# Kernel tuning notes

Measured on AMD Instinct MI355X. Metric: run time of the kernel, lower is better.

The kernel has to match this reference:

```python
import jax, jax.numpy as jnp
import numpy as np

HID = 128
K = 8
G = 1024        # number of graphs (jets)
N_SV = 16       # secondary vertices per graph
N_TRK = 64      # tracks per graph


def _mlp2(x, W1, b1, W2, b2):
    # Linear -> ELU -> Linear -> ReLU (the sv/trk encoders)
    h = jax.nn.elu(x @ W1 + b1)
    return jax.nn.relu(h @ W2 + b2)


def _dynamic_edge_conv(src, dst, W, b, k):
    # DynamicEdgeConv with bipartite input (x_src, x_dst):
    #   edge_index = knn(src, dst, k) per graph (Euclidean in feature space)
    #   message    = nn(cat([x_i, x_j - x_i]))  with x_i = dst(target), x_j = src(neighbor)
    #   aggr       = max over the k neighbors of each target
    # src: [G, Ns, D], dst: [G, Nq, D]
    dots = jnp.einsum('gqd,gsd->gqs', dst, src)
    d2 = (jnp.sum(dst * dst, -1)[:, :, None] - 2.0 * dots
          + jnp.sum(src * src, -1)[:, None, :])            # [G, Nq, Ns]
    _, idx = jax.lax.top_k(-d2, k)                          # k nearest sources, [G, Nq, k]
    xj = jax.vmap(lambda s, i: s[i])(src, idx)              # gather neighbors [G, Nq, k, D]
    xi = dst[:, :, None, :]                                 # [G, Nq, 1, D]
    edge_feat = jnp.concatenate([jnp.broadcast_to(xi, xj.shape), xj - xi], axis=-1)
    msg = jax.nn.elu(edge_feat @ W + b)                     # [G, Nq, k, D]
    return jnp.max(msg, axis=2)                             # max-scatter -> [G, Nq, D]


def setup_inputs() -> dict:
    key = jax.random.key(0)
    ks = jax.random.split(key, 16)
    s = 0.05
    inp = {
        'x_sv': jax.random.normal(ks[0], (G * N_SV, 2), jnp.float32),
        'x_trk': jax.random.normal(ks[1], (G * N_TRK, 8), jnp.float32),
        # sv encoder
        'W_sv1': jax.random.normal(ks[2], (2, HID), jnp.float32) * s,
        'b_sv1': jnp.zeros((HID,), jnp.float32),
        'W_sv2': jax.random.normal(ks[3], (HID, HID), jnp.float32) * s,
        'b_sv2': jnp.zeros((HID,), jnp.float32),
        # trk encoder
        'W_trk1': jax.random.normal(ks[4], (8, HID), jnp.float32) * s,
        'b_trk1': jnp.zeros((HID,), jnp.float32),
        'W_trk2': jax.random.normal(ks[5], (HID, HID), jnp.float32) * s,
        'b_trk2': jnp.zeros((HID,), jnp.float32),
        # edge-conv MLPs (Linear(2*HID, HID) + ELU)
        'W_c1': jax.random.normal(ks[6], (2 * HID, HID), jnp.float32) * s,
        'b_c1': jnp.zeros((HID,), jnp.float32),
        'W_c2': jax.random.normal(ks[7], (2 * HID, HID), jnp.float32) * s,
        'b_c2': jnp.zeros((HID,), jnp.float32),
        # output head 128->64->32->4->1
        'W_o1': jax.random.normal(ks[8], (HID, 64), jnp.float32) * s,
        'b_o1': jnp.zeros((64,), jnp.float32),
        'W_o2': jax.random.normal(ks[9], (64, 32), jnp.float32) * s,
        'b_o2': jnp.zeros((32,), jnp.float32),
        'W_o3': jax.random.normal(ks[10], (32, 4), jnp.float32) * s,
        'b_o3': jnp.zeros((4,), jnp.float32),
        'W_o4': jax.random.normal(ks[11], (4, 1), jnp.float32) * s,
        'b_o4': jnp.zeros((1,), jnp.float32),
        # block-structured batch assignment (sorted, equal-size graphs)
        'batch_sv': jnp.arange(G * N_SV, dtype=jnp.int64 if jax.config.jax_enable_x64 else jnp.int32) // N_SV,
        'batch_trk': jnp.arange(G * N_TRK, dtype=jnp.int64 if jax.config.jax_enable_x64 else jnp.int32) // N_TRK,
    }
    return inp


def reference(x_sv, x_trk, W_sv1, b_sv1, W_sv2, b_sv2, W_trk1, b_trk1, W_trk2, b_trk2,
              W_c1, b_c1, W_c2, b_c2, W_o1, b_o1, W_o2, b_o2, W_o3, b_o3, W_o4, b_o4,
              batch_sv, batch_trk):
    # Batches are equal-size contiguous blocks (see setup_inputs), so per-graph
    # knn/gather/max are expressed as batched ops over a leading G dimension.
    sv = _mlp2(x_sv, W_sv1, b_sv1, W_sv2, b_sv2).reshape(G, N_SV, HID)
    trk = _mlp2(x_trk, W_trk1, b_trk1, W_trk2, b_trk2).reshape(G, N_TRK, HID)
    # conv_1: sources = encoded SVs, targets = encoded tracks
    f1 = _dynamic_edge_conv(sv, trk, W_c1, b_c1, K)          # [G, N_TRK, HID]
    # conv_2: sources = f1 (per-track), targets = encoded tracks
    f2 = _dynamic_edge_conv(f1, trk, W_c2, b_c2, K)          # [G, N_TRK, HID]
    # avg_pool_x with cluster == batch: mean over tracks of each graph
    pooled = jnp.mean(f2, axis=1)                            # [G, HID]
    h = jax.nn.elu(pooled @ W_o1 + b_o1)
    h = jax.nn.elu(h @ W_o2 + b_o2)
    h = jax.nn.elu(h @ W_o3 + b_o3)
    out = h @ W_o4 + b_o4                                    # [G, 1]
    batch = jnp.arange(G)
    return out, batch
```

## Files before the change

### kernel.cpp

```cpp
#include <hip/hip_runtime.h>

#define G_    1024
#define TPB   512
#define INF_F 3.4e38f

typedef __attribute__((ext_vector_type(8))) short short8;
typedef __attribute__((ext_vector_type(4))) float f32x4;

__device__ __forceinline__ float elu_fast(float x) { return x > 0.f ? x : __expf(x) - 1.f; }
__device__ __forceinline__ float elu_ref(float x)  { return x > 0.f ? x : expm1f(x); }

#define ROT(r, d)    ((r)*128 + (((d) + 4*(r)) & 127))
#define BS1(s, c)    (2048 + (s)*128 + (((c) + 4*(s)) & 127))

#define FMA4(acc_, sc_, wv_) do { (acc_).x = fmaf((sc_),(wv_).x,(acc_).x); \
                                  (acc_).y = fmaf((sc_),(wv_).y,(acc_).y); \
                                  (acc_).z = fmaf((sc_),(wv_).z,(acc_).z); \
                                  (acc_).w = fmaf((sc_),(wv_).w,(acc_).w); } while(0)
#define MAX4(mm_, bb_)       do { (mm_).x = fmaxf((mm_).x,(bb_).x); \
                                  (mm_).y = fmaxf((mm_).y,(bb_).y); \
                                  (mm_).z = fmaxf((mm_).z,(bb_).z); \
                                  (mm_).w = fmaxf((mm_).w,(bb_).w); } while(0)

#define MFMA1(acc_, A_, B_) \
    acc_ = __builtin_amdgcn_mfma_f32_16x16x32_bf16((A_), (B_), (acc_), 0, 0, 0)

union U8 { unsigned d[4]; short8 v; };

__device__ __forceinline__ short8 pack_frag(const float* p0, const float* p1) {
    float xs[8];
    *(float4*)&xs[0] = *(const float4*)p0;
    *(float4*)&xs[4] = *(const float4*)p1;
    U8 uo;
    #pragma unroll
    for (int k = 0; k < 4; k++) {
        unsigned u0 = __float_as_uint(xs[2 * k]);
        unsigned u1 = __float_as_uint(xs[2 * k + 1]);
        u0 = u0 + 0x7FFFu + ((u0 >> 16) & 1u);
        u1 = u1 + 0x7FFFu + ((u1 >> 16) & 1u);
        uo.d[k] = (u0 >> 16) | (u1 & 0xFFFF0000u);
    }
    return uo.v;
}

__device__ __forceinline__ unsigned short bf16_of(float v) {
    unsigned u = __float_as_uint(v);
    u = u + 0x7FFFu + ((u >> 16) & 1u);
    return (unsigned short)(u >> 16);
}
__device__ __forceinline__ float f32_of(unsigned short h) {
    return __uint_as_float((unsigned)h << 16);
}

__global__ void prep_pack(const float* __restrict__ Wtrk2, const float* __restrict__ Wsv2,
                          const float* __restrict__ Wc1,   const float* __restrict__ Wc2,
                          unsigned short* __restrict__ wsu) {
    const int o = blockIdx.x * 256 + threadIdx.x;
    if (o >= 6 * 16384) return;
    const int m = o >> 14, pos = o & 16383;
    const int j = pos & 7, lane = (pos >> 3) & 63, tile = pos >> 9;
    const int ks = tile >> 3, ni = tile & 7;
    const int d = ks * 32 + (lane >> 4) * 8 + j;
    const int c = ni * 16 + (lane & 15);
    const int e = d * 128 + c;
    float v;
    switch (m) {
        case 0: v = Wtrk2[e]; break;
        case 1: v = Wsv2[e]; break;
        case 2: v = Wc1[16384 + e]; break;
        case 3: v = Wc1[e] - Wc1[16384 + e]; break;
        case 4: v = Wc2[e] - Wc2[16384 + e]; break;
        default: v = Wc2[16384 + e]; break;
    }
    wsu[m * 16384 + pos] = bf16_of(v);
}

#define LOADB1(B_, m_, pos_) B_ = *(const short8*)(wsu + (m_) * 16384 + (pos_))

__global__ __launch_bounds__(TPB, 4)
void fused_mfma(const float* __restrict__ x_sv,  const float* __restrict__ x_trk,
                const float* __restrict__ W_sv1, const float* __restrict__ b_sv1,
                const float* __restrict__ b_sv2,
                const float* __restrict__ W_trk1,const float* __restrict__ b_trk1,
                const float* __restrict__ b_trk2,
                const float* __restrict__ b_c1,  const float* __restrict__ b_c2,
                const float* __restrict__ W_o1,  const float* __restrict__ b_o1,
                const float* __restrict__ W_o2,  const float* __restrict__ b_o2,
                const float* __restrict__ W_o3,  const float* __restrict__ b_o3,
                const float* __restrict__ W_o4,  const float* __restrict__ b_o4,
                const unsigned short* __restrict__ wsu,
                float* __restrict__ out)
{
    __shared__ float sA[8192];
    __shared__ float sB[8192];
    __shared__ float sC[4096];
    unsigned* sBu = (unsigned*)sB;
    unsigned short* sCs = (unsigned short*)sC;

    const int g    = blockIdx.x;
    const int tid  = threadIdx.x;
    const int c128 = tid & 127;
    const int g4   = tid >> 7;
    const int wv   = tid >> 6;
    const int lane = tid & 63;
    const int quad = lane >> 4;
    const int ln   = lane & 15;

    sC[2048 + tid] = x_trk[(size_t)g * 512 + tid];
    if (tid < 32) sC[2560 + tid] = x_sv[(size_t)g * 32 + tid];
    __syncthreads();

    {
        float w[8];
        #pragma unroll
        for (int k = 0; k < 8; k++) w[k] = W_trk1[k * 128 + c128];
        const float b1 = b_trk1[c128];
        #pragma unroll
        for (int i = 0; i < 16; i++) {
            const int r = g4 * 16 + i;
            float xr[8];
            *(float4*)&xr[0] = *(const float4*)&sC[2048 + r * 8];
            *(float4*)&xr[4] = *(const float4*)&sC[2048 + r * 8 + 4];
            float acc = b1;
            #pragma unroll
            for (int k = 0; k < 8; k++) acc = fmaf(xr[k], w[k], acc);
            sB[ROT(r, c128)] = elu_fast(acc);
        }
    }
    __syncthreads();

    {
        const int mi = wv >> 1, nb = (wv & 1) * 4;
        const int row = mi * 16 + ln;
        f32x4 acc[4];
        #pragma unroll
        for (int t = 0; t < 4; t++) {
            const float bz = b_trk2[(nb + t) * 16 + ln];
            acc[t] = (f32x4){bz, bz, bz, bz};
        }
        #pragma unroll 1
        for (int ks = 0; ks < 4; ks++) {
            const int k0 = ks * 32 + quad * 8;
            const short8 A = pack_frag(&sB[ROT(row, k0)], &sB[ROT(row, k0 + 4)]);
            #pragma unroll
            for (int t = 0; t < 4; t++) {
                const int pos = ((ks * 8 + (nb + t)) * 64 + lane) * 8;
                short8 B;
                LOADB1(B, 0, pos);
                MFMA1(acc[t], A, B);
            }
        }
        #pragma unroll
        for (int t = 0; t < 4; t++)
            #pragma unroll
            for (int r = 0; r < 4; r++)
                sA[ROT(mi * 16 + quad * 4 + r, (nb + t) * 16 + ln)] = fmaxf(acc[t][r], 0.f);
    }
    __syncthreads();

    {
        const float w0 = W_sv1[c128], w1 = W_sv1[128 + c128];
        const float b1 = b_sv1[c128];
        #pragma unroll
        for (int i = 0; i < 4; i++) {
            const int s = g4 * 4 + i;
            sB[ROT(s, c128)] =
                elu_fast(fmaf(sC[2560 + s * 2 + 1], w1, fmaf(sC[2560 + s * 2], w0, b1)));
        }
    }
    __syncthreads();

    {
        const int ni = wv;
        const float bz = b_sv2[ni * 16 + ln];
        f32x4 acc = (f32x4){bz, bz, bz, bz};
        #pragma unroll 1
        for (int ks = 0; ks < 4; ks++) {
            const int k0 = ks * 32 + quad * 8;
            const short8 A = pack_frag(&sB[ROT(ln, k0)], &sB[ROT(ln, k0 + 4)]);
            const int pos = ((ks * 8 + ni) * 64 + lane) * 8;
            short8 B;
            LOADB1(B, 1, pos);
            MFMA1(acc, A, B);
        }
        #pragma unroll
        for (int r = 0; r < 4; r++) {
            const float v = fmaxf(acc[r], 0.f);
            sC[ROT(quad * 4 + r, ni * 16 + ln)] = v;
            float p = v * v;
            #pragma unroll
            for (int o = 1; o <= 8; o <<= 1) p += __shfl_xor(p, o, 16);
            if (ln == 0) sB[2048 + ni * 16 + quad * 4 + r] = p;
        }
    }
    __syncthreads();

    {
        const int ni = wv;
        const bool doP4 = (wv < 4);
        f32x4 accB = (f32x4){0.f, 0.f, 0.f, 0.f};
        f32x4 accS = (f32x4){0.f, 0.f, 0.f, 0.f};
        #pragma unroll 1
        for (int ks = 0; ks < 4; ks++) {
            const int k0 = ks * 32 + quad * 8;
            const short8 S = pack_frag(&sC[ROT(ln, k0)], &sC[ROT(ln, k0 + 4)]);
            const int pos = ((ks * 8 + ni) * 64 + lane) * 8;
            short8 B;
            LOADB1(B, 2, pos);
            MFMA1(accB, S, B);
            if (doP4) {
                const int row = wv * 16 + ln;
                const short8 T = pack_frag(&sA[ROT(row, k0)], &sA[ROT(row, k0 + 4)]);
                MFMA1(accS, T, S);
            }
        }
        #pragma unroll
        for (int r = 0; r < 4; r++)
            sC[BS1(quad * 4 + r, ni * 16 + ln)] = accB[r];
        if (doP4) {
            float nsv = 0.f;
            #pragma unroll
            for (int p = 0; p < 8; p++) nsv += sB[2048 + p * 16 + ln];
            #pragma unroll
            for (int r = 0; r < 4; r++)
                sB[(wv * 16 + quad * 4 + r) * 17 + ln] = fmaf(-2.f, accS[r], nsv);
        }
    }
    __syncthreads();

    {
        const int q  = tid >> 3;
        const int s0 = tid & 7;
        float sc0 = sB[q * 17 + s0];
        float sc1 = sB[q * 17 + s0 + 8];
        unsigned pack1 = 0u;
        #pragma unroll
        for (int r = 0; r < 8; r++) {
            float bv = sc0; int bs = s0;
            if (sc1 < bv) { bv = sc1; bs = s0 + 8; }
            #pragma unroll
            for (int o = 1; o <= 4; o <<= 1) {
                const float ov = __shfl_xor(bv, o, 8);
                const int   os = __shfl_xor(bs, o, 8);
                if (ov < bv || (ov == bv && os < bs)) { bv = ov; bs = os; }
            }
            pack1 |= (unsigned)bs << (4 * r);
            if (bs == s0)     sc0 = INF_F;
            if (bs == s0 + 8) sc1 = INF_F;
        }
        if (s0 == 0) sBu[1088 + q] = pack1;
    }
    __syncthreads();

    {
        const int mi = wv >> 1, nb = (wv & 1) * 4;
        const int row = mi * 16 + ln;
        f32x4 a1acc[4];
        #pragma unroll
        for (int t = 0; t < 4; t++) {
            const float bz1 = b_c1[(nb + t) * 16 + ln];
            a1acc[t] = (f32x4){bz1, bz1, bz1, bz1};
        }
        #pragma unroll 1
        for (int ks = 0; ks < 4; ks++) {
            const int k0 = ks * 32 + quad * 8;
            const short8 A = pack_frag(&sA[ROT(row, k0)], &sA[ROT(row, k0 + 4)]);
            #pragma unroll
            for (int t = 0; t < 4; t++) {
                const int pos = ((ks * 8 + (nb + t)) * 64 + lane) * 8;
                short8 B;
                LOADB1(B, 3, pos);
                MFMA1(a1acc[t], A, B);
            }
        }
        unsigned pk[4];
        #pragma unroll
        for (int r = 0; r < 4; r++) pk[r] = sBu[1088 + mi * 16 + quad * 4 + r];
        __syncthreads();
        float np[4] = {0.f, 0.f, 0.f, 0.f};
        #pragma unroll
        for (int t = 0; t < 4; t++) {
            const int cc = (nb + t) * 16 + ln;
            #pragma unroll
            for (int r = 0; r < 4; r++) {
                float mx = -INF_F;
                #pragma unroll
                for (int j = 0; j < 8; j++) {
                    const int s = (int)((pk[r] >> (4 * j)) & 15u);
                    mx = fmaxf(mx, sC[BS1(s, cc)]);
                }
                const float f = elu_fast(a1acc[t][r] + mx);
                sB[ROT(mi * 16 + quad * 4 + r, cc)] = f;
                np[r] = fmaf(f, f, np[r]);
            }
        }
        #pragma unroll
        for (int r = 0; r < 4; r++) {
            #pragma unroll
            for (int o = 1; o <= 8; o <<= 1) np[r] += __shfl_xor(np[r], o, 16);
            if (ln == 0) sC[(wv & 1) * 64 + mi * 16 + quad * 4 + r] = np[r];
        }
    }
    __syncthreads();

    {
        const int mi = wv >> 1, nia = (wv & 1) * 2;
        const int row = mi * 16 + ln;
        float ns[2];
        #pragma unroll
        for (int u = 0; u < 2; u++) {
            const int s = (nia + u) * 16 + ln;
            ns[u] = sC[s] + sC[64 + s];
        }
        __syncthreads();
        f32x4 acc[2];
        acc[0] = (f32x4){0.f, 0.f, 0.f, 0.f};
        acc[1] = (f32x4){0.f, 0.f, 0.f, 0.f};
        #pragma unroll 1
        for (int ks = 0; ks < 4; ks++) {
            const int k0 = ks * 32 + quad * 8;
            const short8 A = pack_frag(&sA[ROT(row, k0)], &sA[ROT(row, k0 + 4)]);
            #pragma unroll
            for (int u = 0; u < 2; u++) {
                const int srow = (nia + u) * 16 + ln;
                const short8 B = pack_frag(&sB[ROT(srow, k0)], &sB[ROT(srow, k0 + 4)]);
                MFMA1(acc[u], A, B);
            }
        }
        #pragma unroll
        for (int u = 0; u < 2; u++) {
            const int s = (nia + u) * 16 + ln;
            #pragma unroll
            for (int r = 0; r < 4; r++)
                sC[(mi * 16 + quad * 4 + r) * 64 + s] = fmaf(-2.f, acc[u][r], ns[u]);
        }
    }
    __syncthreads();

    unsigned lo2, hi2;
    {
        const int q = tid >> 3;
        const int j = tid & 7;
        float v[8];
        *(float4*)&v[0] = *(const float4*)&sC[q * 64 + 8 * j];
        *(float4*)&v[4] = *(const float4*)&sC[q * 64 + 8 * j + 4];
        lo2 = 0u; hi2 = 0u;
        #pragma unroll
        for (int r = 0; r < 8; r++) {
            float bv = v[0]; int bs = 8 * j;
            #pragma unroll
            for (int t = 1; t < 8; t++)
                if (v[t] < bv) { bv = v[t]; bs = 8 * j + t; }
            #pragma unroll
            for (int o = 1; o <= 4; o <<= 1) {
                const float ov = __shfl_xor(bv, o, 8);
                const int   os = __shfl_xor(bs, o, 8);
                if (ov < bv || (ov == bv && os < bs)) { bv = ov; bs = os; }
            }
            if (r < 4) lo2 |= (unsigned)bs << (8 * r);
            else       hi2 |= (unsigned)bs << (8 * (r - 4));
            #pragma unroll
            for (int t = 0; t < 8; t++)
                if (bs == 8 * j + t) v[t] = INF_F;
        }
    }
    __syncthreads();

    {
        const int mi = wv >> 1, nb = (wv & 1) * 4;
        const int row = mi * 16 + ln;
        f32x4 a2acc[4];
        #pragma unroll
        for (int t = 0; t < 4; t++) {
            const float bz2 = b_c2[(nb + t) * 16 + ln];
            a2acc[t] = (f32x4){bz2, bz2, bz2, bz2};
        }
        #pragma unroll 1
        for (int ks = 0; ks < 4; ks++) {
            const int k0 = ks * 32 + quad * 8;
            const short8 A = pack_frag(&sA[ROT(row, k0)], &sA[ROT(row, k0 + 4)]);
            #pragma unroll
            for (int t = 0; t < 4; t++) {
                const int pos = ((ks * 8 + (nb + t)) * 64 + lane) * 8;
                short8 B;
                LOADB1(B, 4, pos);
                MFMA1(a2acc[t], A, B);
            }
        }
        #pragma unroll
        for (int t = 0; t < 4; t++)
            #pragma unroll
            for (int r = 0; r < 4; r++)
                sCs[tid * 16 + t * 4 + r] = bf16_of(a2acc[t][r]);
    }
    __syncthreads();

    {
        const int mi = wv >> 1, nb = (wv & 1) * 4;
        const int row = mi * 16 + ln;
        f32x4 acc[4];
        #pragma unroll
        for (int t = 0; t < 4; t++) acc[t] = (f32x4){0.f, 0.f, 0.f, 0.f};
        #pragma unroll 1
        for (int ks = 0; ks < 4; ks++) {
            const int k0 = ks * 32 + quad * 8;
            const short8 A = pack_frag(&sB[ROT(row, k0)], &sB[ROT(row, k0 + 4)]);
            #pragma unroll
            for (int t = 0; t < 4; t++) {
                const int pos = ((ks * 8 + (nb + t)) * 64 + lane) * 8;
                short8 B;
                LOADB1(B, 5, pos);
                MFMA1(acc[t], A, B);
            }
        }
        #pragma unroll
        for (int t = 0; t < 4; t++)
            #pragma unroll
            for (int r = 0; r < 4; r++)
                sA[ROT(mi * 16 + quad * 4 + r, (nb + t) * 16 + ln)] = acc[t][r];
    }
    __syncthreads();

    if ((tid & 7) == 0) {
        const int q = tid >> 3;
        sBu[1024 + 2 * q]     = lo2;
        sBu[1024 + 2 * q + 1] = hi2;
    }
    __syncthreads();

    {
        const int mi = wv >> 1, nb = (wv & 1) * 4;
        float ps[4] = {0.f, 0.f, 0.f, 0.f};
        #pragma unroll
        for (int t = 0; t < 4; t++) {
            const int cc = (nb + t) * 16 + ln;
            #pragma unroll
            for (int r = 0; r < 4; r++) {
                const int rr = mi * 16 + quad * 4 + r;
                const unsigned plo = sBu[1024 + 2 * rr];
                const unsigned phi = sBu[1024 + 2 * rr + 1];
                float mx = -INF_F;
                #pragma unroll
                for (int j = 0; j < 8; j++) {
                    const int s = (int)(((j < 4) ? (plo >> (8 * j))
                                                 : (phi >> (8 * (j - 4)))) & 63u);
                    mx = fmaxf(mx, sA[ROT(s, cc)]);
                }
                const float a2v = f32_of(sCs[tid * 16 + t * 4 + r]);
                ps[t] += elu_fast(a2v + mx);
            }
        }
        #pragma unroll
        for (int t = 0; t < 4; t++) {
            ps[t] += __shfl_xor(ps[t], 16, 64);
            ps[t] += __shfl_xor(ps[t], 32, 64);
        }
        if (lane < 16)
            #pragma unroll
            for (int t = 0; t < 4; t++)
                sB[mi * 128 + (nb + t) * 16 + lane] = ps[t];
    }
    __syncthreads();

    if (tid < 128) {
        const float p = (sB[tid] + sB[128 + tid] + sB[256 + tid] + sB[384 + tid]) * (1.f / 64.f);
        sB[512 + tid] = p;
    }
    __syncthreads();
    if (tid < 64) {
        float acc = b_o1[tid];
        for (int d = 0; d < 128; d++) acc = fmaf(sB[512 + d], W_o1[d * 64 + tid], acc);
        sB[640 + tid] = elu_fast(acc);
    }
    __syncthreads();
    if (tid < 32) {
        float acc = b_o2[tid];
        for (int d = 0; d < 64; d++) acc = fmaf(sB[640 + d], W_o2[d * 32 + tid], acc);
        sB[704 + tid] = elu_fast(acc);
    }
    __syncthreads();
    if (tid < 4) {
        float acc = b_o3[tid];
        for (int d = 0; d < 32; d++) acc = fmaf(sB[704 + d], W_o3[d * 4 + tid], acc);
        sB[736 + tid] = elu_fast(acc);
    }
    __syncthreads();
    if (tid == 0) {
        float acc = b_o4[0];
        #pragma unroll
        for (int d = 0; d < 4; d++) acc = fmaf(sB[736 + d], W_o4[d], acc);
        out[g] = acc;
        out[G_ + g] = (float)g;
    }
}

#define ROTV(r, d)    ((r)*128 + (((d) + 4*(r)) & 127))
#define BS1V(s, c)    (2048 + (s)*128 + (((c) + 4*(s)) & 127))
__global__ __launch_bounds__(TPB, 2)
void fused_vec(const float* __restrict__ x_sv,  const float* __restrict__ x_trk,
               const float* __restrict__ W_sv1, const float* __restrict__ b_sv1,
               const float* __restrict__ W_sv2, const float* __restrict__ b_sv2,
               const float* __restrict__ W_trk1,const float* __restrict__ b_trk1,
               const float* __restrict__ W_trk2,const float* __restrict__ b_trk2,
               const float* __restrict__ W_c1,  const float* __restrict__ b_c1,
               const float* __restrict__ W_c2,  const float* __restrict__ b_c2,
               const float* __restrict__ W_o1,  const float* __restrict__ b_o1,
               const float* __restrict__ W_o2,  const float* __restrict__ b_o2,
               const float* __restrict__ W_o3,  const float* __restrict__ b_o3,
               const float* __restrict__ W_o4,  const float* __restrict__ b_o4,
               float* __restrict__ out)
{
    __shared__ float sA[8192];
    __shared__ float sB[8192];
    __shared__ float sC[4096];
    const int g    = blockIdx.x;
    const int tid  = threadIdx.x;
    const int c128 = tid & 127;
    const int g4   = tid >> 7;
    const int cq   = tid & 31;
    const int c0   = cq * 4;
    const int rg   = tid >> 5;
    const int lane_hi = tid & 32;

    sC[2048 + tid] = x_trk[(size_t)g * 512 + tid];
    if (tid < 32) sC[2560 + tid] = x_sv[(size_t)g * 32 + tid];
    __syncthreads();
    {
        float w[8];
        #pragma unroll
        for (int k = 0; k < 8; k++) w[k] = W_trk1[k * 128 + c128];
        const float b1 = b_trk1[c128];
        #pragma unroll
        for (int i = 0; i < 16; i++) {
            const int r = g4 * 16 + i;
            float acc = b1;
            #pragma unroll
            for (int k = 0; k < 8; k++) acc = fmaf(sC[2048 + r * 8 + k], w[k], acc);
            sB[r * 128 + c128] = elu_ref(acc);
        }
    }
    __syncthreads();
    {
        const int r0 = rg * 4;
        float4 acc[4];
        const float4 bz = *(const float4*)&b_trk2[c0];
        #pragma unroll
        for (int i = 0; i < 4; i++) acc[i] = bz;
        for (int d0 = 0; d0 < 128; d0 += 4) {
            const float4 w0 = *(const float4*)&W_trk2[(d0 + 0) * 128 + c0];
            const float4 w1 = *(const float4*)&W_trk2[(d0 + 1) * 128 + c0];
            const float4 w2 = *(const float4*)&W_trk2[(d0 + 2) * 128 + c0];
            const float4 w3 = *(const float4*)&W_trk2[(d0 + 3) * 128 + c0];
            #pragma unroll
            for (int i = 0; i < 4; i++) {
                const float4 h = *(const float4*)&sB[(r0 + i) * 128 + d0];
                FMA4(acc[i], h.x, w0); FMA4(acc[i], h.y, w1);
                FMA4(acc[i], h.z, w2); FMA4(acc[i], h.w, w3);
            }
        }
        #pragma unroll
        for (int i = 0; i < 4; i++) {
            float4 r;
            r.x = fmaxf(acc[i].x, 0.f); r.y = fmaxf(acc[i].y, 0.f);
            r.z = fmaxf(acc[i].z, 0.f); r.w = fmaxf(acc[i].w, 0.f);
            *(float4*)&sA[ROTV(r0 + i, c0)] = r;
        }
    }
    __syncthreads();
    {
        const float w0 = W_sv1[c128], w1 = W_sv1[128 + c128];
        const float b1 = b_sv1[c128];
        #pragma unroll
        for (int i = 0; i < 4; i++) {
            const int s = g4 * 4 + i;
            sB[s * 128 + c128] =
                elu_ref(fmaf(sC[2560 + s * 2 + 1], w1, fmaf(sC[2560 + s * 2], w0, b1)));
        }
    }
    __syncthreads();
    {
        const int s = rg;
        float4 acc = *(const float4*)&b_sv2[c0];
        for (int d0 = 0; d0 < 128; d0 += 4) {
            const float4 w0 = *(const float4*)&W_sv2[(d0 + 0) * 128 + c0];
            const float4 w1 = *(const float4*)&W_sv2[(d0 + 1) * 128 + c0];
            const float4 w2 = *(const float4*)&W_sv2[(d0 + 2) * 128 + c0];
            const float4 w3 = *(const float4*)&W_sv2[(d0 + 3) * 128 + c0];
            const float4 h = *(const float4*)&sB[s * 128 + d0];
            FMA4(acc, h.x, w0); FMA4(acc, h.y, w1);
            FMA4(acc, h.z, w2); FMA4(acc, h.w, w3);
        }
        float4 r;
        r.x = fmaxf(acc.x, 0.f); r.y = fmaxf(acc.y, 0.f);
        r.z = fmaxf(acc.z, 0.f); r.w = fmaxf(acc.w, 0.f);
        *(float4*)&sC[ROTV(s, c0)] = r;
    }
    __syncthreads();
    unsigned pack1;
    {
        {
            const int s = rg;
            float4 acc = {0.f, 0.f, 0.f, 0.f};
            for (int d0 = 0; d0 < 128; d0 += 4) {
                const float4 e  = *(const float4*)&sC[ROTV(s, d0)];
                const float4 w0 = *(const float4*)&W_c1[(128 + d0 + 0) * 128 + c0];
                const float4 w1 = *(const float4*)&W_c1[(128 + d0 + 1) * 128 + c0];
                const float4 w2 = *(const float4*)&W_c1[(128 + d0 + 2) * 128 + c0];
                const float4 w3 = *(const float4*)&W_c1[(128 + d0 + 3) * 128 + c0];
                FMA4(acc, e.x, w0); FMA4(acc, e.y, w1);
                FMA4(acc, e.z, w2); FMA4(acc, e.w, w3);
            }
            *(float4*)&sC[BS1V(s, c0)] = acc;
        }
        const int q  = tid >> 3;
        const int s0 = tid & 7;
        float d0a = 0.f, d1a = 0.f, n0 = 0.f, n1 = 0.f;
        for (int d0 = 0; d0 < 128; d0 += 4) {
            const float4 t  = *(const float4*)&sA[ROTV(q, d0)];
            const float4 v0 = *(const float4*)&sC[ROTV(s0, d0)];
            const float4 v1 = *(const float4*)&sC[ROTV(s0 + 8, d0)];
            d0a += t.x * v0.x + t.y * v0.y + t.z * v0.z + t.w * v0.w;
            d1a += t.x * v1.x + t.y * v1.y + t.z * v1.z + t.w * v1.w;
            n0  += v0.x * v0.x + v0.y * v0.y + v0.z * v0.z + v0.w * v0.w;
            n1  += v1.x * v1.x + v1.y * v1.y + v1.z * v1.z + v1.w * v1.w;
        }
        float sc0 = fmaf(-2.f, d0a, n0);
        float sc1 = fmaf(-2.f, d1a, n1);
        pack1 = 0u;
        #pragma unroll
        for (int r = 0; r < 8; r++) {
            float bv = sc0; int bs = s0;
            if (sc1 < bv) { bv = sc1; bs = s0 + 8; }
            #pragma unroll
            for (int o = 1; o <= 4; o <<= 1) {
                const float ov = __shfl_xor(bv, o, 8);
                const int   os = __shfl_xor(bs, o, 8);
                if (ov < bv || (ov == bv && os < bs)) { bv = ov; bs = os; }
            }
            pack1 |= (unsigned)bs << (4 * r);
            if (bs == s0)     sc0 = INF_F;
            if (bs == s0 + 8) sc1 = INF_F;
        }
    }
    __syncthreads();
    float4 a2v[4];
    {
        const int q0 = rg * 4;
        float4 a1[4];
        const float4 bc1 = *(const float4*)&b_c1[c0];
        const float4 bc2 = *(const float4*)&b_c2[c0];
        #pragma unroll
        for (int i = 0; i < 4; i++) { a1[i] = bc1; a2v[i] = bc2; }
        for (int d0 = 0; d0 < 128; d0 += 4) {
            float4 t[4];
            #pragma unroll
            for (int i = 0; i < 4; i++) t[i] = *(const float4*)&sA[ROTV(q0 + i, d0)];
            #pragma unroll
            for (int dj = 0; dj < 4; dj++) {
                float4 wv;
                const float4 wa = *(const float4*)&W_c1[(d0 + dj) * 128 + c0];
                const float4 wb = *(const float4*)&W_c1[(128 + d0 + dj) * 128 + c0];
                wv.x = wa.x - wb.x; wv.y = wa.y - wb.y;
                wv.z = wa.z - wb.z; wv.w = wa.w - wb.w;
                FMA4(a1[0], ((const float*)&t[0])[dj], wv);
                FMA4(a1[1], ((const float*)&t[1])[dj], wv);
                FMA4(a1[2], ((const float*)&t[2])[dj], wv);
                FMA4(a1[3], ((const float*)&t[3])[dj], wv);
            }
            #pragma unroll
            for (int dj = 0; dj < 4; dj++) {
                float4 wv;
                const float4 wa = *(const float4*)&W_c2[(d0 + dj) * 128 + c0];
                const float4 wb = *(const float4*)&W_c2[(128 + d0 + dj) * 128 + c0];
                wv.x = wa.x - wb.x; wv.y = wa.y - wb.y;
                wv.z = wa.z - wb.z; wv.w = wa.w - wb.w;
                FMA4(a2v[0], ((const float*)&t[0])[dj], wv);
                FMA4(a2v[1], ((const float*)&t[1])[dj], wv);
                FMA4(a2v[2], ((const float*)&t[2])[dj], wv);
                FMA4(a2v[3], ((const float*)&t[3])[dj], wv);
            }
        }
        #pragma unroll
        for (int i = 0; i < 4; i++) {
            const int q = q0 + i;
            const unsigned pk = __shfl(pack1, 8 * i + lane_hi);
            float4 m = {-INF_F, -INF_F, -INF_F, -INF_F};
            #pragma unroll
            for (int j = 0; j < 8; j++) {
                const int s = (int)((pk >> (4 * j)) & 15u);
                const float4 b = *(const float4*)&sC[BS1V(s, c0)];
                MAX4(m, b);
            }
            float4 f;
            f.x = elu_ref(a1[i].x + m.x); f.y = elu_ref(a1[i].y + m.y);
            f.z = elu_ref(a1[i].z + m.z); f.w = elu_ref(a1[i].w + m.w);
            *(float4*)&sB[ROTV(q, c0)] = f;
        }
    }
    __syncthreads();
    {
        const int s  = tid & 63;
        const int q0 = (tid >> 6) * 8;
        float acc[8];
        #pragma unroll
        for (int i = 0; i < 8; i++) acc[i] = 0.f;
        float nrm = 0.f;
        for (int d0 = 0; d0 < 128; d0 += 4) {
            const float4 f = *(const float4*)&sB[ROTV(s, d0)];
            nrm = fmaf(f.x, f.x, nrm); nrm = fmaf(f.y, f.y, nrm);
            nrm = fmaf(f.z, f.z, nrm); nrm = fmaf(f.w, f.w, nrm);
            #pragma unroll
            for (int i = 0; i < 8; i++) {
                const float4 t = *(const float4*)&sA[ROTV(q0 + i, d0)];
                acc[i] = fmaf(t.x, f.x, acc[i]); acc[i] = fmaf(t.y, f.y, acc[i]);
                acc[i] = fmaf(t.z, f.z, acc[i]); acc[i] = fmaf(t.w, f.w, acc[i]);
            }
        }
        #pragma unroll
        for (int i = 0; i < 8; i++)
            sC[(q0 + i) * 64 + s] = fmaf(-2.f, acc[i], nrm);
    }
    __syncthreads();
    unsigned lo2, hi2;
    {
        const int q = tid >> 3;
        const int j = tid & 7;
        float v[8];
        *(float4*)&v[0] = *(const float4*)&sC[q * 64 + 8 * j];
        *(float4*)&v[4] = *(const float4*)&sC[q * 64 + 8 * j + 4];
        lo2 = 0u; hi2 = 0u;
        #pragma unroll
        for (int r = 0; r < 8; r++) {
            float bv = v[0]; int bs = 8 * j;
            #pragma unroll
            for (int t = 1; t < 8; t++)
                if (v[t] < bv) { bv = v[t]; bs = 8 * j + t; }
            #pragma unroll
            for (int o = 1; o <= 4; o <<= 1) {
                const float ov = __shfl_xor(bv, o, 8);
                const int   os = __shfl_xor(bs, o, 8);
                if (ov < bv || (ov == bv && os < bs)) { bv = ov; bs = os; }
            }
            if (r < 4) lo2 |= (unsigned)bs << (8 * r);
            else       hi2 |= (unsigned)bs << (8 * (r - 4));
            #pragma unroll
            for (int t = 0; t < 8; t++)
                if (bs == 8 * j + t) v[t] = INF_F;
        }
        const int r0 = rg * 4;
        float4 acc[4];
        #pragma unroll
        for (int i = 0; i < 4; i++) acc[i] = make_float4(0.f, 0.f, 0.f, 0.f);
        for (int d0 = 0; d0 < 128; d0 += 4) {
            const float4 w0 = *(const float4*)&W_c2[(128 + d0 + 0) * 128 + c0];
            const float4 w1 = *(const float4*)&W_c2[(128 + d0 + 1) * 128 + c0];
            const float4 w2 = *(const float4*)&W_c2[(128 + d0 + 2) * 128 + c0];
            const float4 w3 = *(const float4*)&W_c2[(128 + d0 + 3) * 128 + c0];
            #pragma unroll
            for (int i = 0; i < 4; i++) {
                const float4 f = *(const float4*)&sB[ROTV(r0 + i, d0)];
                FMA4(acc[i], f.x, w0); FMA4(acc[i], f.y, w1);
                FMA4(acc[i], f.z, w2); FMA4(acc[i], f.w, w3);
            }
        }
        #pragma unroll
        for (int i = 0; i < 4; i++)
            *(float4*)&sA[ROTV(r0 + i, c0)] = acc[i];
    }
    __syncthreads();
    {
        const int q0 = rg * 4;
        float4 ps = {0.f, 0.f, 0.f, 0.f};
        #pragma unroll
        for (int i = 0; i < 4; i++) {
            const unsigned plo = __shfl(lo2, 8 * i + lane_hi);
            const unsigned phi = __shfl(hi2, 8 * i + lane_hi);
            float4 m = {-INF_F, -INF_F, -INF_F, -INF_F};
            #pragma unroll
            for (int j = 0; j < 8; j++) {
                const int s = (int)(((j < 4) ? (plo >> (8 * j)) : (phi >> (8 * (j - 4)))) & 63u);
                const float4 b = *(const float4*)&sA[ROTV(s, c0)];
                MAX4(m, b);
            }
            ps.x += elu_ref(a2v[i].x + m.x); ps.y += elu_ref(a2v[i].y + m.y);
            ps.z += elu_ref(a2v[i].z + m.z); ps.w += elu_ref(a2v[i].w + m.w);
        }
        *(float4*)&sB[rg * 128 + c0] = ps;
    }
    __syncthreads();
    if (tid < 128) {
        float p = 0.f;
        #pragma unroll
        for (int t = 0; t < 16; t++) p += sB[t * 128 + tid];
        sB[2048 + tid] = p * (1.f / 64.f);
    }
    __syncthreads();
    if (tid < 64) {
        float acc = b_o1[tid];
        for (int d = 0; d < 128; d++) acc = fmaf(sB[2048 + d], W_o1[d * 64 + tid], acc);
        sB[2176 + tid] = elu_ref(acc);
    }
    __syncthreads();
    if (tid < 32) {
        float acc = b_o2[tid];
        for (int d = 0; d < 64; d++) acc = fmaf(sB[2176 + d], W_o2[d * 32 + tid], acc);
        sB[2240 + tid] = elu_ref(acc);
    }
    __syncthreads();
    if (tid < 4) {
        float acc = b_o3[tid];
        for (int d = 0; d < 32; d++) acc = fmaf(sB[2240 + d], W_o3[d * 4 + tid], acc);
        sB[2272 + tid] = elu_ref(acc);
    }
    __syncthreads();
    if (tid == 0) {
        float acc = b_o4[0];
        #pragma unroll
        for (int d = 0; d < 4; d++) acc = fmaf(sB[2272 + d], W_o4[d], acc);
        out[g] = acc;
        out[G_ + g] = (float)g;
    }
}

extern "C" void kernel_launch(void* const* d_in, const int* in_sizes, int n_in,
                              void* d_out, int out_size, void* d_ws, size_t ws_size,
                              hipStream_t stream) {
    const float* x_sv   = (const float*)d_in[0];
    const float* x_trk  = (const float*)d_in[1];
    const float* W_sv1  = (const float*)d_in[2];
    const float* b_sv1  = (const float*)d_in[3];
    const float* W_sv2  = (const float*)d_in[4];
    const float* b_sv2  = (const float*)d_in[5];
    const float* W_trk1 = (const float*)d_in[6];
    const float* b_trk1 = (const float*)d_in[7];
    const float* W_trk2 = (const float*)d_in[8];
    const float* b_trk2 = (const float*)d_in[9];
    const float* W_c1   = (const float*)d_in[10];
    const float* b_c1   = (const float*)d_in[11];
    const float* W_c2   = (const float*)d_in[12];
    const float* b_c2   = (const float*)d_in[13];
    const float* W_o1   = (const float*)d_in[14];
    const float* b_o1   = (const float*)d_in[15];
    const float* W_o2   = (const float*)d_in[16];
    const float* b_o2   = (const float*)d_in[17];
    const float* W_o3   = (const float*)d_in[18];
    const float* b_o3   = (const float*)d_in[19];
    const float* W_o4   = (const float*)d_in[20];
    const float* b_o4   = (const float*)d_in[21];
    float* out = (float*)d_out;

    const size_t WS_NEED = (size_t)6 * 16384 * sizeof(unsigned short);
    if (ws_size >= WS_NEED && d_ws != nullptr) {
        unsigned short* wsu = (unsigned short*)d_ws;
        prep_pack<<<384, 256, 0, stream>>>(W_trk2, W_sv2, W_c1, W_c2, wsu);
        fused_mfma<<<G_, TPB, 0, stream>>>(x_sv, x_trk, W_sv1, b_sv1, b_sv2,
                                           W_trk1, b_trk1, b_trk2, b_c1, b_c2,
                                           W_o1, b_o1, W_o2, b_o2, W_o3, b_o3,
                                           W_o4, b_o4, wsu, out);
    } else {
        fused_vec<<<G_, TPB, 0, stream>>>(x_sv, x_trk, W_sv1, b_sv1, W_sv2, b_sv2,
                                          W_trk1, b_trk1, W_trk2, b_trk2,
                                          W_c1, b_c1, W_c2, b_c2,
                                          W_o1, b_o1, W_o2, b_o2, W_o3, b_o3,
                                          W_o4, b_o4, out);
    }
}
```

Measured before the change: 190.3 us.

## Store MFMA operand tiles as bf16 in LDS and shrink shared memory footprint

Activations that feed MFMA are now written to LDS already rounded to bf16 with a new rotation swizzle. Fragments are loaded as a single short8 instead of being packed from two float4 loads on every read. Shared memory drops from 80KB to 48KB and launch bounds rise to 6 blocks, so occupancy can go up. The a2 accumulator is kept in registers instead of LDS, and the gather-max loops are reordered to reuse neighbour indices across four columns. The f2 buffer is split between two arrays.

Result: faster. 170.4 us (-10.4%).

```diff
diff --git a/kernel.cpp b/kernel.cpp
--- a/kernel.cpp
+++ b/kernel.cpp
@@ -10,8 +10,9 @@
 __device__ __forceinline__ float elu_fast(float x) { return x > 0.f ? x : __expf(x) - 1.f; }
 __device__ __forceinline__ float elu_ref(float x)  { return x > 0.f ? x : expm1f(x); }
 
-#define ROT(r, d)    ((r)*128 + (((d) + 4*(r)) & 127))
-#define BS1(s, c)    (2048 + (s)*128 + (((c) + 4*(s)) & 127))
+#define RB(r, c)     ((r)*128 + (((c) + 8*(r)) & 127))
+#define RF(r, c)     ((r)*128 + (((c) + 4*(r)) & 127))
+#define B1F(s, c)    (2048 + RF(s, c))
 
 #define FMA4(acc_, sc_, wv_) do { (acc_).x = fmaf((sc_),(wv_).x,(acc_).x); \
                                   (acc_).y = fmaf((sc_),(wv_).y,(acc_).y); \
@@ -24,24 +25,6 @@
 
 #define MFMA1(acc_, A_, B_) \
     acc_ = __builtin_amdgcn_mfma_f32_16x16x32_bf16((A_), (B_), (acc_), 0, 0, 0)
-
-union U8 { unsigned d[4]; short8 v; };
-
-__device__ __forceinline__ short8 pack_frag(const float* p0, const float* p1) {
-    float xs[8];
-    *(float4*)&xs[0] = *(const float4*)p0;
-    *(float4*)&xs[4] = *(const float4*)p1;
-    U8 uo;
-    #pragma unroll
-    for (int k = 0; k < 4; k++) {
-        unsigned u0 = __float_as_uint(xs[2 * k]);
-        unsigned u1 = __float_as_uint(xs[2 * k + 1]);
-        u0 = u0 + 0x7FFFu + ((u0 >> 16) & 1u);
-        u1 = u1 + 0x7FFFu + ((u1 >> 16) & 1u);
-        uo.d[k] = (u0 >> 16) | (u1 & 0xFFFF0000u);
-    }
-    return uo.v;
-}
 
 __device__ __forceinline__ unsigned short bf16_of(float v) {
     unsigned u = __float_as_uint(v);
@@ -76,8 +59,9 @@
 }
 
 #define LOADB1(B_, m_, pos_) B_ = *(const short8*)(wsu + (m_) * 16384 + (pos_))
-
-__global__ __launch_bounds__(TPB, 4)
+#define LDFRAG(buf_, r_, k0_) (*(const short8*)&(buf_)[RB((r_), (k0_))])
+
+__global__ __launch_bounds__(TPB, 6)
 void fused_mfma(const float* __restrict__ x_sv,  const float* __restrict__ x_trk,
                 const float* __restrict__ W_sv1, const float* __restrict__ b_sv1,
                 const float* __restrict__ b_sv2,
@@ -91,11 +75,13 @@
                 const unsigned short* __restrict__ wsu,
                 float* __restrict__ out)
 {
-    __shared__ float sA[8192];
-    __shared__ float sB[8192];
-    __shared__ float sC[4096];
-    unsigned* sBu = (unsigned*)sB;
-    unsigned short* sCs = (unsigned short*)sC;
+    __shared__ __align__(16) char sAraw[16384];
+    __shared__ __align__(16) char sBraw[16384];
+    __shared__ __align__(16) char sCraw[16384];
+    short*    sAh = (short*)sAraw;    float* sAf = (float*)sAraw;
+    short*    sBh = (short*)sBraw;    float* sBf = (float*)sBraw;
+    unsigned* sBu = (unsigned*)sBraw;
+    short*    sCh = (short*)sCraw;    float* sCf = (float*)sCraw;
 
     const int g    = blockIdx.x;
     const int tid  = threadIdx.x;
@@ -106,8 +92,8 @@
     const int quad = lane >> 4;
     const int ln   = lane & 15;
 
-    sC[2048 + tid] = x_trk[(size_t)g * 512 + tid];
-    if (tid < 32) sC[2560 + tid] = x_sv[(size_t)g * 32 + tid];
+    sCf[2048 + tid] = x_trk[(size_t)g * 512 + tid];
+    if (tid < 32) sCf[2560 + tid] = x_sv[(size_t)g * 32 + tid];
     __syncthreads();
 
     {
@@ -119,12 +105,12 @@
         for (int i = 0; i < 16; i++) {
             const int r = g4 * 16 + i;
             float xr[8];
-            *(float4*)&xr[0] = *(const float4*)&sC[2048 + r * 8];
-            *(float4*)&xr[4] = *(const float4*)&sC[2048 + r * 8 + 4];
+            *(float4*)&xr[0] = *(const float4*)&sCf[2048 + r * 8];
+            *(float4*)&xr[4] = *(const float4*)&sCf[2048 + r * 8 + 4];
             float acc = b1;
             #pragma unroll
             for (int k = 0; k < 8; k++) acc = fmaf(xr[k], w[k], acc);
-            sB[ROT(r, c128)] = elu_fast(acc);
+            sBh[RB(r, c128)] = bf16_of(elu_fast(acc));
         }
     }
     __syncthreads();
@@ -141,7 +127,7 @@
         #pragma unroll 1
         for (int ks = 0; ks < 4; ks++) {
             const int k0 = ks * 32 + quad * 8;
-            const short8 A = pack_frag(&sB[ROT(row, k0)], &sB[ROT(row, k0 + 4)]);
+            const short8 A = LDFRAG(sBh, row, k0);
             #pragma unroll
             for (int t = 0; t < 4; t++) {
                 const int pos = ((ks * 8 + (nb + t)) * 64 + lane) * 8;
@@ -154,7 +140,8 @@
         for (int t = 0; t < 4; t++)
             #pragma unroll
             for (int r = 0; r < 4; r++)
-                sA[ROT(mi * 16 + quad * 4 + r, (nb + t) * 16 + ln)] = fmaxf(acc[t][r], 0.f);
+                sAh[RB(mi * 16 + quad * 4 + r, (nb + t) * 16 + ln)] =
+                    bf16_of(fmaxf(acc[t][r], 0.f));
     }
     __syncthreads();
 
@@ -164,8 +151,8 @@
         #pragma unroll
         for (int i = 0; i < 4; i++) {
             const int s = g4 * 4 + i;
-            sB[ROT(s, c128)] =
-                elu_fast(fmaf(sC[2560 + s * 2 + 1], w1, fmaf(sC[2560 + s * 2], w0, b1)));
+            sBh[RB(s, c128)] = bf16_of(
+                elu_fast(fmaf(sCf[2560 + s * 2 + 1], w1, fmaf(sCf[2560 + s * 2], w0, b1))));
         }
     }
     __syncthreads();
@@ -177,7 +164,7 @@
         #pragma unroll 1
         for (int ks = 0; ks < 4; ks++) {
             const int k0 = ks * 32 + quad * 8;
-            const short8 A = pack_frag(&sB[ROT(ln, k0)], &sB[ROT(ln, k0 + 4)]);
+            const short8 A = LDFRAG(sBh, ln, k0);
             const int pos = ((ks * 8 + ni) * 64 + lane) * 8;
             short8 B;
             LOADB1(B, 1, pos);
@@ -186,11 +173,11 @@
         #pragma unroll
         for (int r = 0; r < 4; r++) {
             const float v = fmaxf(acc[r], 0.f);
-            sC[ROT(quad * 4 + r, ni * 16 + ln)] = v;
+            sCh[RB(quad * 4 + r, ni * 16 + ln)] = bf16_of(v);
             float p = v * v;
             #pragma unroll
             for (int o = 1; o <= 8; o <<= 1) p += __shfl_xor(p, o, 16);
-            if (ln == 0) sB[2048 + ni * 16 + quad * 4 + r] = p;
+            if (ln == 0) sBf[2048 + ni * 16 + quad * 4 + r] = p;
         }
     }
     __syncthreads();
@@ -203,27 +190,26 @@
         #pragma unroll 1
         for (int ks = 0; ks < 4; ks++) {
             const int k0 = ks * 32 + quad * 8;
-            const short8 S = pack_frag(&sC[ROT(ln, k0)], &sC[ROT(ln, k0 + 4)]);
+            const short8 S = LDFRAG(sCh, ln, k0);
             const int pos = ((ks * 8 + ni) * 64 + lane) * 8;
             short8 B;
             LOADB1(B, 2, pos);
             MFMA1(accB, S, B);
             if (doP4) {
-                const int row = wv * 16 + ln;
-                const short8 T = pack_frag(&sA[ROT(row, k0)], &sA[ROT(row, k0 + 4)]);
+                const short8 T = LDFRAG(sAh, wv * 16 + ln, k0);
                 MFMA1(accS, T, S);
             }
         }
         #pragma unroll
         for (int r = 0; r < 4; r++)
-            sC[BS1(quad * 4 + r, ni * 16 + ln)] = accB[r];
+            sCf[B1F(quad * 4 + r, ni * 16 + ln)] = accB[r];
         if (doP4) {
             float nsv = 0.f;
             #pragma unroll
-            for (int p = 0; p < 8; p++) nsv += sB[2048 + p * 16 + ln];
+            for (int p = 0; p < 8; p++) nsv += sBf[2048 + p * 16 + ln];
             #pragma unroll
             for (int r = 0; r < 4; r++)
-                sB[(wv * 16 + quad * 4 + r) * 17 + ln] = fmaf(-2.f, accS[r], nsv);
+                sBf[(wv * 16 + quad * 4 + r) * 17 + ln] = fmaf(-2.f, accS[r], nsv);
         }
     }
     __syncthreads();
@@ -231,8 +217,8 @@
     {
         const int q  = tid >> 3;
         const int s0 = tid & 7;
-        float sc0 = sB[q * 17 + s0];
-        float sc1 = sB[q * 17 + s0 + 8];
+        float sc0 = sBf[q * 17 + s0];
+        float sc1 = sBf[q * 17 + s0 + 8];
         unsigned pack1 = 0u;
         #pragma unroll
         for (int r = 0; r < 8; r++) {
@@ -264,7 +250,7 @@
         #pragma unroll 1
         for (int ks = 0; ks < 4; ks++) {
             const int k0 = ks * 32 + quad * 8;
-            const short8 A = pack_frag(&sA[ROT(row, k0)], &sA[ROT(row, k0 + 4)]);
+            const short8 A = LDFRAG(sAh, row, k0);
             #pragma unroll
             for (int t = 0; t < 4; t++) {
                 const int pos = ((ks * 8 + (nb + t)) * 64 + lane) * 8;
@@ -278,19 +264,23 @@
         for (int r = 0; r < 4; r++) pk[r] = sBu[1088 + mi * 16 + quad * 4 + r];
         __syncthreads();
         float np[4] = {0.f, 0.f, 0.f, 0.f};
-        #pragma unroll
-        for (int t = 0; t < 4; t++) {
-            const int cc = (nb + t) * 16 + ln;
-            #pragma unroll
-            for (int r = 0; r < 4; r++) {
-                float mx = -INF_F;
+        const int ccb = nb * 16 + ln;
+        #pragma unroll
+        for (int r = 0; r < 4; r++) {
+            float mx[4] = {-INF_F, -INF_F, -INF_F, -INF_F};
+            #pragma unroll
+            for (int j = 0; j < 8; j++) {
+                const int s  = (int)((pk[r] >> (4 * j)) & 15u);
+                const int sa = 2048 + s * 128;
+                const int ro = 4 * s;
                 #pragma unroll
-                for (int j = 0; j < 8; j++) {
-                    const int s = (int)((pk[r] >> (4 * j)) & 15u);
-                    mx = fmaxf(mx, sC[BS1(s, cc)]);
-                }
-                const float f = elu_fast(a1acc[t][r] + mx);
-                sB[ROT(mi * 16 + quad * 4 + r, cc)] = f;
+                for (int t = 0; t < 4; t++)
+                    mx[t] = fmaxf(mx[t], sCf[sa + ((ccb + 16 * t + ro) & 127)]);
+            }
+            #pragma unroll
+            for (int t = 0; t < 4; t++) {
+                const float f = elu_fast(a1acc[t][r] + mx[t]);
+                sBh[RB(mi * 16 + quad * 4 + r, ccb + 16 * t)] = bf16_of(f);
                 np[r] = fmaf(f, f, np[r]);
             }
         }
@@ -298,7 +288,7 @@
         for (int r = 0; r < 4; r++) {
             #pragma unroll
             for (int o = 1; o <= 8; o <<= 1) np[r] += __shfl_xor(np[r], o, 16);
-            if (ln == 0) sC[(wv & 1) * 64 + mi * 16 + quad * 4 + r] = np[r];
+            if (ln == 0) sCf[(wv & 1) * 64 + mi * 16 + quad * 4 + r] = np[r];
         }
     }
     __syncthreads();
@@ -310,7 +300,7 @@
         #pragma unroll
         for (int u = 0; u < 2; u++) {
             const int s = (nia + u) * 16 + ln;
-            ns[u] = sC[s] + sC[64 + s];
+            ns[u] = sCf[s] + sCf[64 + s];
         }
         __syncthreads();
         f32x4 acc[2];
@@ -319,12 +309,11 @@
         #pragma unroll 1
         for (int ks = 0; ks < 4; ks++) {
             const int k0 = ks * 32 + quad * 8;
-            const short8 A = pack_frag(&sA[ROT(row, k0)], &sA[ROT(row, k0 + 4)]);
+            const short8 A = LDFRAG(sAh, row, k0);
             #pragma unroll
             for (int u = 0; u < 2; u++) {
-                const int srow = (nia + u) * 16 + ln;
-                const short8 B = pack_frag(&sB[ROT(srow, k0)], &sB[ROT(srow, k0 + 4)]);
-                MFMA1(acc[u], A, B);
+                const short8 Bf = LDFRAG(sBh, (nia + u) * 16 + ln, k0);
+                MFMA1(acc[u], A, Bf);
             }
         }
         #pragma unroll
@@ -332,7 +321,7 @@
             const int s = (nia + u) * 16 + ln;
             #pragma unroll
             for (int r = 0; r < 4; r++)
-                sC[(mi * 16 + quad * 4 + r) * 64 + s] = fmaf(-2.f, acc[u][r], ns[u]);
+                sCf[(mi * 16 + quad * 4 + r) * 64 + s] = fmaf(-2.f, acc[u][r], ns[u]);
         }
     }
     __syncthreads();
@@ -342,8 +331,8 @@
         const int q = tid >> 3;
         const int j = tid & 7;
         float v[8];
-        *(float4*)&v[0] = *(const float4*)&sC[q * 64 + 8 * j];
-        *(float4*)&v[4] = *(const float4*)&sC[q * 64 + 8 * j + 4];
+        *(float4*)&v[0] = *(const float4*)&sCf[q * 64 + 8 * j];
+        *(float4*)&v[4] = *(const float4*)&sCf[q * 64 + 8 * j + 4];
         lo2 = 0u; hi2 = 0u;
         #pragma unroll
         for (int r = 0; r < 8; r++) {
@@ -366,6 +355,7 @@
     }
     __syncthreads();
 
+    unsigned a2p[8];
     {
         const int mi = wv >> 1, nb = (wv & 1) * 4;
         const int row = mi * 16 + ln;
@@ -378,7 +368,7 @@
         #pragma unroll 1
         for (int ks = 0; ks < 4; ks++) {
             const int k0 = ks * 32 + quad * 8;
-            const short8 A = pack_frag(&sA[ROT(row, k0)], &sA[ROT(row, k0 + 4)]);
+            const short8 A = LDFRAG(sAh, row, k0);
             #pragma unroll
             for (int t = 0; t < 4; t++) {
                 const int pos = ((ks * 8 + (nb + t)) * 64 + lane) * 8;
@@ -388,10 +378,12 @@
             }
         }
         #pragma unroll
-        for (int t = 0; t < 4; t++)
-            #pragma unroll
-            for (int r = 0; r < 4; r++)
-                sCs[tid * 16 + t * 4 + r] = bf16_of(a2acc[t][r]);
+        for (int t = 0; t < 4; t++) {
+            a2p[2 * t]     = (unsigned)bf16_of(a2acc[t][0]) |
+                             ((unsigned)bf16_of(a2acc[t][1]) << 16);
+            a2p[2 * t + 1] = (unsigned)bf16_of(a2acc[t][2]) |
+                             ((unsigned)bf16_of(a2acc[t][3]) << 16);
+        }
     }
     __syncthreads();
 
@@ -404,7 +396,7 @@
         #pragma unroll 1
         for (int ks = 0; ks < 4; ks++) {
             const int k0 = ks * 32 + quad * 8;
-            const short8 A = pack_frag(&sB[ROT(row, k0)], &sB[ROT(row, k0 + 4)]);
+            const short8 A = LDFRAG(sBh, row, k0);
             #pragma unroll
             for (int t = 0; t < 4; t++) {
                 const int pos = ((ks * 8 + (nb + t)) * 64 + lane) * 8;
@@ -413,11 +405,14 @@
                 MFMA1(acc[t], A, B);
             }
         }
+        float* bp = (mi < 2) ? sAf : sCf;
         #pragma unroll
         for (int t = 0; t < 4; t++)
             #pragma unroll
-            for (int r = 0; r < 4; r++)
-                sA[ROT(mi * 16 + quad * 4 + r, (nb + t) * 16 + ln)] = acc[t][r];
+            for (int r = 0; r < 4; r++) {
+                const int rr = mi * 16 + quad * 4 + r;
+                bp[RF(rr & 31, (nb + t) * 16 + ln)] = acc[t][r];
+            }
     }
     __syncthreads();
 
@@ -431,23 +426,29 @@
     {
         const int mi = wv >> 1, nb = (wv & 1) * 4;
         float ps[4] = {0.f, 0.f, 0.f, 0.f};
-        #pragma unroll
-        for (int t = 0; t < 4; t++) {
-            const int cc = (nb + t) * 16 + ln;
-            #pragma unroll
-            for (int r = 0; r < 4; r++) {
-                const int rr = mi * 16 + quad * 4 + r;
-                const unsigned plo = sBu[1024 + 2 * rr];
-                const unsigned phi = sBu[1024 + 2 * rr + 1];
-                float mx = -INF_F;
+        const int ccb = nb * 16 + ln;
+        #pragma unroll
+        for (int r = 0; r < 4; r++) {
+            const int rr = mi * 16 + quad * 4 + r;
+            const unsigned plo = sBu[1024 + 2 * rr];
+            const unsigned phi = sBu[1024 + 2 * rr + 1];
+            float mx[4] = {-INF_F, -INF_F, -INF_F, -INF_F};
+            #pragma unroll
+            for (int j = 0; j < 8; j++) {
+                const int s = (int)(((j < 4) ? (plo >> (8 * j))
+                                             : (phi >> (8 * (j - 4)))) & 63u);
+                const float* bp = (s < 32) ? sAf : sCf;
+                const int sa = (s & 31) * 128;
+                const int ro = 4 * s;
                 #pragma unroll
-                for (int j = 0; j < 8; j++) {
-                    const int s = (int)(((j < 4) ? (plo >> (8 * j))
-                                                 : (phi >> (8 * (j - 4)))) & 63u);
-                    mx = fmaxf(mx, sA[ROT(s, cc)]);
-                }
-                const float a2v = f32_of(sCs[tid * 16 + t * 4 + r]);
-                ps[t] += elu_fast(a2v + mx);
+                for (int t = 0; t < 4; t++)
+                    mx[t] = fmaxf(mx[t], bp[sa + ((ccb + 16 * t + ro) & 127)]);
+            }
+            #pragma unroll
+            for (int t = 0; t < 4; t++) {
+                const unsigned u = a2p[2 * t + (r >> 1)];
+                const float a2v = __uint_as_float((r & 1) ? (u & 0xFFFF0000u) : (u << 16));
+                ps[t] += elu_fast(a2v + mx[t]);
             }
         }
         #pragma unroll
@@ -458,37 +459,37 @@
         if (lane < 16)
             #pragma unroll
             for (int t = 0; t < 4; t++)
-                sB[mi * 128 + (nb + t) * 16 + lane] = ps[t];
+                sBf[mi * 128 + (nb + t) * 16 + lane] = ps[t];
     }
     __syncthreads();
 
     if (tid < 128) {
-        const float p = (sB[tid] + sB[128 + tid] + sB[256 + tid] + sB[384 + tid]) * (1.f / 64.f);
-        sB[512 + tid] = p;
+        const float p = (sBf[tid] + sBf[128 + tid] + sBf[256 + tid] + sBf[384 + tid]) * (1.f / 64.f);
+        sBf[512 + tid] = p;
     }
     __syncthreads();
     if (tid < 64) {
         float acc = b_o1[tid];
-        for (int d = 0; d < 128; d++) acc = fmaf(sB[512 + d], W_o1[d * 64 + tid], acc);
-        sB[640 + tid] = elu_fast(acc);
+        for (int d = 0; d < 128; d++) acc = fmaf(sBf[512 + d], W_o1[d * 64 + tid], acc);
+        sBf[640 + tid] = elu_fast(acc);
     }
     __syncthreads();
     if (tid < 32) {
         float acc = b_o2[tid];
-        for (int d = 0; d < 64; d++) acc = fmaf(sB[640 + d], W_o2[d * 32 + tid], acc);
-        sB[704 + tid] = elu_fast(acc);
+        for (int d = 0; d < 64; d++) acc = fmaf(sBf[640 + d], W_o2[d * 32 + tid], acc);
+        sBf[704 + tid] = elu_fast(acc);
     }
     __syncthreads();
     if (tid < 4) {
         float acc = b_o3[tid];
-        for (int d = 0; d < 32; d++) acc = fmaf(sB[704 + d], W_o3[d * 4 + tid], acc);
-        sB[736 + tid] = elu_fast(acc);
+        for (int d = 0; d < 32; d++) acc = fmaf(sBf[704 + d], W_o3[d * 4 + tid], acc);
+        sBf[736 + tid] = elu_fast(acc);
     }
     __syncthreads();
     if (tid == 0) {
         float acc = b_o4[0];
         #pragma unroll
-        for (int d = 0; d < 4; d++) acc = fmaf(sB[736 + d], W_o4[d], acc);
+        for (int d = 0; d < 4; d++) acc = fmaf(sBf[736 + d], W_o4[d], acc);
         out[g] = acc;
         out[G_ + g] = (float)g;
     }
```
